# Optimization experiments

Measured on AMD Instinct MI355X. Metric: run time of the kernel, lower is better.

Reference implementation:

```python
import jax, jax.numpy as jnp
import numpy as np

B, S = 2, 1024
NH, NKV, HD = 32, 8, 128
Q_DIM, KV_DIM = NH * HD, NKV * HD
LEVEL = 256
ROPE_BASE = 10000.0


def fq_sym(x, level=LEVEL):
    # symmetric per-tensor fake quant with straight-through estimator
    qp = level // 2 - 1
    s = jnp.maximum(jax.lax.stop_gradient(jnp.max(jnp.abs(x))) / qp, 1e-8)
    q = jnp.clip(jnp.round(x / s), -qp, qp) * s
    return x + jax.lax.stop_gradient(q - x)


def fq_asym(x, level=LEVEL):
    # asymmetric (unsigned) fake quant for values in [0, 1]
    qp = level - 1
    s = jnp.maximum(jax.lax.stop_gradient(jnp.max(x)) / qp, 1e-8)
    q = jnp.clip(jnp.round(x / s), 0, qp) * s
    return x + jax.lax.stop_gradient(q - x)


def rope_tables(seq_len, dim):
    inv_freq = 1.0 / (ROPE_BASE ** (jnp.arange(0, dim, 2, dtype=jnp.float32) / dim))
    freqs = jnp.arange(seq_len, dtype=jnp.float32)[:, None] * inv_freq[None, :]  # [S, HD/2]
    emb = jnp.concatenate([freqs, freqs], axis=-1)  # [S, HD]
    return jnp.cos(emb), jnp.sin(emb)


def rotate_half(x):
    x1, x2 = jnp.split(x, 2, axis=-1)
    return jnp.concatenate([-x2, x1], axis=-1)


def setup_inputs() -> dict:
    key = jax.random.key(0)
    k1, k2, k3, k4 = jax.random.split(key, 4)
    d = Q_DIM + 2 * KV_DIM
    x = jax.random.normal(k1, (B, S, d), dtype=jnp.float32)
    w_qkv = jax.random.normal(k2, (d, d), dtype=jnp.float32) * (d ** -0.5)
    w_o = jax.random.normal(k3, (Q_DIM, Q_DIM), dtype=jnp.float32) * (Q_DIM ** -0.5)
    core_slope = jnp.float32(0.25)
    causal_mask = jnp.where(
        jnp.triu(jnp.ones((S, S), dtype=bool), k=1), jnp.float32(-1e9), jnp.float32(0.0)
    )[None, None]
    return {"x": x, "w_qkv": w_qkv, "w_o": w_o, "core_slope": core_slope,
            "causal_mask": causal_mask}


def reference(x, w_qkv, w_o, core_slope, causal_mask):
    qkv = jnp.einsum("bsd,ed->bse", x, w_qkv)  # Linear, no bias
    q = qkv[..., :Q_DIM].reshape(B, S, NH, HD).transpose(0, 2, 1, 3)
    k = qkv[..., Q_DIM:Q_DIM + KV_DIM].reshape(B, S, NKV, HD).transpose(0, 2, 1, 3)
    v = qkv[..., Q_DIM + KV_DIM:].reshape(B, S, NKV, HD).transpose(0, 2, 1, 3)
    q, k, v = fq_sym(q), fq_sym(k), fq_sym(v)
    cos, sin = rope_tables(S, HD)
    cos, sin = cos[None, None], sin[None, None]  # [1,1,S,HD]
    q = q * cos + rotate_half(q) * sin
    k = k * cos + rotate_half(k) * sin
    groups = NH // NKV
    if groups > 1:
        k = jnp.repeat(k, groups, axis=1)  # [B,NH,S,HD]
        v = jnp.repeat(v, groups, axis=1)
    scale = HD ** -0.5
    scores = jnp.einsum("bhqd,bhkd->bhqk", q, k) * scale
    scores = scores + causal_mask
    attn = jnp.clip(0.5 + core_slope * scores, 0.0, 1.0)  # UniAffineCore -> [0,1]
    attn = fq_asym(attn)
    out = jnp.einsum("bhqk,bhkd->bhqd", attn, v)
    out = fq_sym(out)
    out = out.transpose(0, 2, 1, 3).reshape(B, S, Q_DIM)
    out = jnp.einsum("bsd,ed->bse", out, w_o)
    return fq_sym(out)
```

## Files before the change

kernel.cpp:

```cpp
#include <hip/hip_runtime.h>
#include <stdint.h>

#define BB   2
#define SS   1024
#define NH   32
#define NKV  8
#define HD   128
#define DQ   4096
#define DKV  1024
#define DD   6144
#define MM   2048
#define SCALE 0.08838834764831845f

typedef __attribute__((ext_vector_type(8))) short short8;
typedef __attribute__((ext_vector_type(4))) float f4;

__device__ __forceinline__ float b2f(unsigned short b) {
    union { unsigned int u; float f; } v; v.u = ((unsigned int)b) << 16; return v.f;
}
__device__ __forceinline__ unsigned short f2b(float f) {
    union { float f; unsigned int u; } v; v.f = f;
    unsigned int u = v.u;
    unsigned int r = u + 0x7fffu + ((u >> 16) & 1u);
    return (unsigned short)(r >> 16);
}
__device__ __forceinline__ float fqs(float x, float s) {
    return fminf(fmaxf(rintf(x / s), -127.f), 127.f) * s;
}

typedef const unsigned int __attribute__((address_space(1)))* gas_ptr;
typedef unsigned int __attribute__((address_space(3)))* las_ptr;
__device__ __forceinline__ void gl_lds16(const void* g, void* l) {
    __builtin_amdgcn_global_load_lds((gas_ptr)(uintptr_t)g,
                                     (las_ptr)(unsigned int)(uintptr_t)l, 16, 0, 0);
}

__global__ void detect_kernel(const unsigned short* __restrict__ x, float* scal) {
    __shared__ float w[4];
    int tid = threadIdx.x;
    float m = 0.f;
    for (int i = tid; i < 65536; i += 256) m = fmaxf(m, fabsf(b2f(x[i])));
#pragma unroll
    for (int off = 32; off > 0; off >>= 1) m = fmaxf(m, __shfl_down(m, off));
    if ((tid & 63) == 0) w[tid >> 6] = m;
    __syncthreads();
    if (tid == 0) {
        float mm = fmaxf(fmaxf(w[0], w[1]), fmaxf(w[2], w[3]));
        scal[6] = (mm > 1e4f) ? 1.0f : 0.0f;
    }
}

__global__ void slope_kernel(const unsigned short* __restrict__ sp, float* scal) {
    if (threadIdx.x == 0)
        scal[7] = (scal[6] > 0.5f) ? ((const float*)sp)[0] : b2f(sp[0]);
}

__global__ void convert_split_kernel(const unsigned short* __restrict__ src,
                                     unsigned short* __restrict__ hi,
                                     unsigned short* __restrict__ lo,
                                     const float* __restrict__ scal) {
    size_t t = (size_t)blockIdx.x * 256 + threadIdx.x;
    float v[8] __attribute__((aligned(16)));
    if (scal[6] > 0.5f) {
        const float* s = (const float*)src + t * 8;
        *(float4*)(v)     = *(const float4*)(s);
        *(float4*)(v + 4) = *(const float4*)(s + 4);
    } else {
        unsigned short u[8] __attribute__((aligned(16)));
        *(uint4*)u = *(const uint4*)(src + t * 8);
#pragma unroll
        for (int i = 0; i < 8; i++) v[i] = b2f(u[i]);
    }
    unsigned short h8[8] __attribute__((aligned(16)));
    unsigned short l8[8] __attribute__((aligned(16)));
#pragma unroll
    for (int i = 0; i < 8; i++) {
        unsigned short h = f2b(v[i]);
        h8[i] = h;
        l8[i] = f2b(v[i] - b2f(h));
    }
    *(uint4*)(hi + t * 8) = *(uint4*)h8;
    *(uint4*)(lo + t * 8) = *(uint4*)l8;
}

template<int NT, int MODE>
__global__ __launch_bounds__(256, 2)
void gemm_hilo_kernel(const unsigned short* __restrict__ Ah,
                      const unsigned short* __restrict__ Al,
                      const unsigned short* __restrict__ Bh,
                      const unsigned short* __restrict__ Bl,
                      float* __restrict__ C,
                      int M, int N, int K,
                      float* __restrict__ scal)
{
    constexpr int PA    = 128 * 32;
    constexpr int OAL   = PA;
    constexpr int OBH   = (NT == 3) ? 2 * PA : PA;
    constexpr int OBL   = OBH + PA;
    constexpr int BUFSH = OBL + PA;
    __shared__ unsigned short lds[2 * BUFSH];
    __shared__ float wred[4];

    const int tid = threadIdx.x;
    const int bn = blockIdx.x << 7;
    const int bm = blockIdx.y << 7;
    const int wave = tid >> 6, lane = tid & 63;
    const int wm = (wave >> 1) << 6, wn = (wave & 1) << 6;
    const int lm = lane & 15, quad = lane >> 4;
    const int qx = quad ^ ((lm >> 1) & 3);

    const f4 z = {0.f, 0.f, 0.f, 0.f};
    f4 acc[4][4];
#pragma unroll
    for (int i = 0; i < 4; i++)
#pragma unroll
        for (int j = 0; j < 4; j++) acc[i][j] = z;

    const int r0 = tid >> 2;
    const int cs = ((tid & 3) ^ ((r0 >> 1) & 3)) * 8;
    const size_t ra0 = (size_t)(bm + r0) * K + cs;
    const size_t ra1 = (size_t)(bm + r0 + 64) * K + cs;
    const size_t rb0 = (size_t)(bn + r0) * K + cs;
    const size_t rb1 = (size_t)(bn + r0 + 64) * K + cs;
    const int l0 = tid * 8, l1 = (tid + 256) * 8;

    auto stage = [&](int bsel, int k0) {
        unsigned short* L = lds + bsel * BUFSH;
        gl_lds16(Ah + ra0 + k0, L + l0);
        gl_lds16(Ah + ra1 + k0, L + l1);
        if (NT == 3) {
            gl_lds16(Al + ra0 + k0, L + OAL + l0);
            gl_lds16(Al + ra1 + k0, L + OAL + l1);
        }
        gl_lds16(Bh + rb0 + k0, L + OBH + l0);
        gl_lds16(Bh + rb1 + k0, L + OBH + l1);
        gl_lds16(Bl + rb0 + k0, L + OBL + l0);
        gl_lds16(Bl + rb1 + k0, L + OBL + l1);
    };

    auto compute = [&](int bsel) {
        const unsigned short* L = lds + bsel * BUFSH;
        short8 a_h[4], b_h[4], b_l[4];
        short8 a_l[(NT == 3) ? 4 : 1];
#pragma unroll
        for (int t = 0; t < 4; t++) {
            int ro = (wm + t * 16 + lm) * 32 + qx * 8;
            a_h[t] = *(const short8*)(L + ro);
            if (NT == 3) a_l[t] = *(const short8*)(L + OAL + ro);
        }
#pragma unroll
        for (int t = 0; t < 4; t++) {
            int ro = (wn + t * 16 + lm) * 32 + qx * 8;
            b_h[t] = *(const short8*)(L + OBH + ro);
            b_l[t] = *(const short8*)(L + OBL + ro);
        }
#pragma unroll
        for (int i = 0; i < 4; i++)
#pragma unroll
            for (int j = 0; j < 4; j++) {
                acc[i][j] = __builtin_amdgcn_mfma_f32_16x16x32_bf16(a_h[i], b_h[j], acc[i][j], 0, 0, 0);
                if (NT == 3)
                    acc[i][j] = __builtin_amdgcn_mfma_f32_16x16x32_bf16(a_l[i], b_h[j], acc[i][j], 0, 0, 0);
                acc[i][j] = __builtin_amdgcn_mfma_f32_16x16x32_bf16(a_h[i], b_l[j], acc[i][j], 0, 0, 0);
            }
    };

#define WAITV do { if (NT == 3) asm volatile("s_waitcnt vmcnt(8)" ::: "memory"); \
                   else         asm volatile("s_waitcnt vmcnt(6)" ::: "memory"); } while (0)
#define WAIT0 asm volatile("s_waitcnt vmcnt(0)" ::: "memory")
#define SCHED0 __builtin_amdgcn_sched_barrier(0)
#define RBAR  __builtin_amdgcn_s_barrier()

    const int nt = K >> 5;
    stage(0, 0);
    stage(1, 32);
    for (int t = 0; t + 2 < nt; ++t) {
        WAITV;
        RBAR; SCHED0;
        compute(t & 1);
        SCHED0; RBAR; SCHED0;
        stage(t & 1, (t + 2) << 5);
    }
    WAITV;  RBAR; SCHED0; compute(nt & 1);
    WAIT0;  RBAR; SCHED0; compute((nt - 1) & 1);

#undef WAITV
#undef WAIT0
#undef SCHED0
#undef RBAR

    float mult = 1.f;
    if (MODE == 1) mult = fmaxf(scal[4] / 127.f, 1e-8f);
    float amax = 0.f;
#pragma unroll
    for (int i = 0; i < 4; i++)
#pragma unroll
        for (int j = 0; j < 4; j++)
#pragma unroll
            for (int r = 0; r < 4; r++) {
                float v = acc[i][j][r] * mult;
                amax = fmaxf(amax, fabsf(v));
                size_t row = (size_t)(bm + wm + i * 16 + quad * 4 + r);
                size_t col = (size_t)(bn + wn + j * 16 + lm);
                C[row * (size_t)N + col] = v;
            }
#pragma unroll
    for (int off = 32; off > 0; off >>= 1) amax = fmaxf(amax, __shfl_down(amax, off));
    if (lane == 0) wred[wave] = amax;
    __syncthreads();
    if (tid == 0) {
        float m = fmaxf(fmaxf(wred[0], wred[1]), fmaxf(wred[2], wred[3]));
        int slot = (MODE == 0) ? ((bn < 4096) ? 0 : ((bn < 5120) ? 1 : 2)) : 5;
        atomicMax((unsigned int*)(scal + slot), __float_as_uint(m));
    }
}

__global__ void quant_rope_hilo_kernel(const float* __restrict__ qkv,
                                       unsigned short* __restrict__ Qh,
                                       unsigned short* __restrict__ Ql,
                                       unsigned short* __restrict__ Kh,
                                       unsigned short* __restrict__ Kl,
                                       unsigned short* __restrict__ Vc,
                                       const float* __restrict__ scal)
{
    int t = blockIdx.x * 256 + threadIdx.x;
    int f = t * 8;
    int r = f / DD;
    int c = f - r * DD;
    int b = r >> 10, sp = r & 1023;
    const float* src = qkv + (size_t)r * DD + c;
    float x[8] __attribute__((aligned(16)));
    *(float4*)(x)     = *(const float4*)(src);
    *(float4*)(x + 4) = *(const float4*)(src + 4);

    if (c < 5120) {
        float s; int d; unsigned short *dh, *dl;
        if (c < 4096) {
            s = fmaxf(scal[0] / 127.f, 1e-8f);
            int head = c >> 7; d = c & 127;
            size_t off = (((size_t)(b * NH + head) * SS + sp) << 7) + d;
            dh = Qh + off; dl = Ql + off;
        } else {
            int cc = c - 4096;
            s = fmaxf(scal[1] / 127.f, 1e-8f);
            int head = cc >> 7; d = cc & 127;
            size_t off = (((size_t)(b * NKV + head) * SS + sp) << 7) + d;
            dh = Kh + off; dl = Kl + off;
        }
        int cp = (d < 64) ? (c + 64) : (c - 64);
        float sgn = (d < 64) ? -1.f : 1.f;
        const float* psrc = qkv + (size_t)r * DD + cp;
        float p[8] __attribute__((aligned(16)));
        *(float4*)(p)     = *(const float4*)(psrc);
        *(float4*)(p + 4) = *(const float4*)(psrc + 4);
        unsigned short h8[8] __attribute__((aligned(16)));
        unsigned short l8[8] __attribute__((aligned(16)));
#pragma unroll
        for (int i = 0; i < 8; i++) {
            float xq = fqs(x[i], s);
            float pq = fqs(p[i], s);
            int fi = (d + i) & 63;
            float inv = expf((float)fi * -0.14391156831212787f);
            float ang = (float)sp * inv;
            float sn, cs;
            sincosf(ang, &sn, &cs);
            float o = xq * cs + sgn * pq * sn;
            unsigned short hb = f2b(o);
            h8[i] = hb;
            l8[i] = f2b(o - b2f(hb));
        }
        *(uint4*)(dh) = *(uint4*)h8;
        *(uint4*)(dl) = *(uint4*)l8;
    } else {
        int cc = c - 5120;
        float s = fmaxf(scal[2] / 127.f, 1e-8f);
        int head = cc >> 7, d = cc & 127;
        unsigned short* dst = Vc + (((size_t)(b * NKV + head) * SS + sp) << 7) + d;
        unsigned short o8[8] __attribute__((aligned(16)));
#pragma unroll
        for (int i = 0; i < 8; i++) {
            float code = fminf(fmaxf(rintf(x[i] / s), -127.f), 127.f);
            o8[i] = f2b(code);
        }
        *(uint4*)(dst) = *(uint4*)o8;
    }
}

__global__ void vtrans_kernel(const unsigned short* __restrict__ Vc,
                              unsigned short* __restrict__ Vt)
{
    __shared__ __attribute__((aligned(16))) unsigned short L[64][72];
    const int dtile = blockIdx.x;
    const int ktile = blockIdx.y;
    const int bh    = blockIdx.z;
    const int tid = threadIdx.x;
#pragma unroll
    for (int it = 0; it < 2; it++) {
        int lin = it * 256 + tid;
        int row = lin >> 3, c8 = (lin & 7) * 8;
        *(uint4*)&L[row][c8] =
            *(const uint4*)(Vc + ((size_t)bh * SS + ktile * 64 + row) * HD + dtile * 64 + c8);
    }
    __syncthreads();
#pragma unroll
    for (int it = 0; it < 2; it++) {
        int lin = it * 256 + tid;
        int dr = lin >> 3, k8 = (lin & 7) * 8;
        unsigned short o8[8] __attribute__((aligned(16)));
#pragma unroll
        for (int i = 0; i < 8; i++) o8[i] = L[k8 + i][dr];
        *(uint4*)(Vt + ((size_t)bh * HD + dtile * 64 + dr) * SS + ktile * 64 + k8) = *(uint4*)o8;
    }
}

template<int PASS>
__global__ __launch_bounds__(256, 2)
void attn_mfma_kernel(const unsigned short* __restrict__ Qh,
                      const unsigned short* __restrict__ Ql,
                      const unsigned short* __restrict__ Kh,
                      const unsigned short* __restrict__ Kl,
                      const unsigned short* __restrict__ Vt,
                      float* __restrict__ O,
                      float* __restrict__ scal)
{
    __shared__ __attribute__((aligned(16))) unsigned short Ps[PASS ? 4 : 1][16][72];
    __shared__ float wred[4];
    const int x = blockIdx.x;
    const int qc = x & 15, h = (x >> 4) & 31, b = x >> 9;
    const int hk = h >> 2;
    const int tid = threadIdx.x;
    const int wave = tid >> 6, lane = tid & 63;
    const int lm = lane & 15, quad = lane >> 4;
    const float coef = scal[7] * SCALE;
    float s_a = 1.f, s_av = 1.f;
    if (PASS) {
        s_a = fmaxf(scal[3] / 255.f, 1e-8f);
        float s_v = fmaxf(scal[2] / 127.f, 1e-8f);
        s_av = s_a * s_v;
    }

    const size_t qbase = ((size_t)((b * NH + h) * SS) + qc * 64 + wave * 16 + lm) * HD + quad * 8;
    short8 qh[4], ql[4];
#pragma unroll
    for (int kk = 0; kk < 4; kk++) {
        qh[kk] = *(const short8*)(Qh + qbase + kk * 32);
        ql[kk] = *(const short8*)(Ql + qbase + kk * 32);
    }
    const size_t kbase = (size_t)((b * NKV + hk) * SS) * HD + quad * 8;
    const size_t vbase = (size_t)((b * NKV + hk) * HD) * SS + quad * 8;

    const f4 z = {0.f, 0.f, 0.f, 0.f};
    f4 oacc[8];
    if (PASS) {
#pragma unroll
        for (int j2 = 0; j2 < 8; j2++) oacc[j2] = z;
    }
    float amax = 0.f;
    const int qg = qc * 64 + wave * 16 + quad * 4;

    for (int kt = 0; kt <= qc; kt++) {
        f4 acc[4];
#pragma unroll
        for (int j = 0; j < 4; j++) acc[j] = z;
        __builtin_amdgcn_s_setprio(1);
#pragma unroll
        for (int j = 0; j < 4; j++) {
            const size_t kb = kbase + (size_t)(kt * 64 + j * 16 + lm) * HD;
#pragma unroll
            for (int kk = 0; kk < 4; kk++) {
                short8 kh8 = *(const short8*)(Kh + kb + kk * 32);
                short8 kl8 = *(const short8*)(Kl + kb + kk * 32);
                acc[j] = __builtin_amdgcn_mfma_f32_16x16x32_bf16(qh[kk], kh8, acc[j], 0, 0, 0);
                acc[j] = __builtin_amdgcn_mfma_f32_16x16x32_bf16(ql[kk], kh8, acc[j], 0, 0, 0);
                acc[j] = __builtin_amdgcn_mfma_f32_16x16x32_bf16(qh[kk], kl8, acc[j], 0, 0, 0);
            }
        }
        __builtin_amdgcn_s_setprio(0);
        const bool diag = (kt == qc);
#pragma unroll
        for (int j = 0; j < 4; j++) {
            int kg = kt * 64 + j * 16 + lm;
#pragma unroll
            for (int r = 0; r < 4; r++) {
                bool ok = (!diag) || (kg <= qg + r);
                float a = 0.5f + coef * acc[j][r];
                a = fminf(fmaxf(a, 0.f), 1.f);
                if (PASS == 0) {
                    if (ok) amax = fmaxf(amax, a);
                } else {
                    float cd = ok ? fminf(rintf(a / s_a), 255.f) : 0.f;
                    Ps[wave][quad * 4 + r][j * 16 + lm] = f2b(cd);
                }
            }
        }
        if (PASS) {
            short8 pa0 = *(const short8*)&Ps[wave][lm][quad * 8];
            short8 pa1 = *(const short8*)&Ps[wave][lm][32 + quad * 8];
            __builtin_amdgcn_s_setprio(1);
#pragma unroll
            for (int j2 = 0; j2 < 8; j2++) {
                const unsigned short* vp = Vt + vbase + (size_t)(j2 * 16 + lm) * SS + kt * 64;
                short8 v0 = *(const short8*)(vp);
                short8 v1 = *(const short8*)(vp + 32);
                oacc[j2] = __builtin_amdgcn_mfma_f32_16x16x32_bf16(pa0, v0, oacc[j2], 0, 0, 0);
                oacc[j2] = __builtin_amdgcn_mfma_f32_16x16x32_bf16(pa1, v1, oacc[j2], 0, 0, 0);
            }
            __builtin_amdgcn_s_setprio(0);
        }
    }

    if (PASS == 0) {
#pragma unroll
        for (int off = 32; off > 0; off >>= 1) amax = fmaxf(amax, __shfl_down(amax, off));
        if (lane == 0) wred[wave] = amax;
        __syncthreads();
        if (tid == 0) {
            float m = fmaxf(fmaxf(wred[0], wred[1]), fmaxf(wred[2], wred[3]));
            atomicMax((unsigned int*)(scal + 3), __float_as_uint(m));
        }
    } else {
        float am = 0.f;
        const size_t orow = (size_t)(b * SS + qc * 64 + wave * 16 + quad * 4);
#pragma unroll
        for (int j2 = 0; j2 < 8; j2++)
#pragma unroll
            for (int r = 0; r < 4; r++) {
                float v = oacc[j2][r] * s_av;
                am = fmaxf(am, fabsf(v));
                O[(orow + r) * DQ + h * HD + j2 * 16 + lm] = v;
            }
#pragma unroll
        for (int off = 32; off > 0; off >>= 1) am = fmaxf(am, __shfl_down(am, off));
        if (lane == 0) wred[wave] = am;
        __syncthreads();
        if (tid == 0) {
            float m = fmaxf(fmaxf(wred[0], wred[1]), fmaxf(wred[2], wred[3]));
            atomicMax((unsigned int*)(scal + 4), __float_as_uint(m));
        }
    }
}

__global__ void quant_o_codes_kernel(const float* __restrict__ O,
                                     const float* __restrict__ scal,
                                     unsigned short* __restrict__ Oq)
{
    size_t t = (size_t)blockIdx.x * 256 + threadIdx.x;
    float s = fmaxf(scal[4] / 127.f, 1e-8f);
    float4 v = *(const float4*)(O + t * 4);
    unsigned short o[4] __attribute__((aligned(8)));
    o[0] = f2b(fminf(fmaxf(rintf(v.x / s), -127.f), 127.f));
    o[1] = f2b(fminf(fmaxf(rintf(v.y / s), -127.f), 127.f));
    o[2] = f2b(fminf(fmaxf(rintf(v.z / s), -127.f), 127.f));
    o[3] = f2b(fminf(fmaxf(rintf(v.w / s), -127.f), 127.f));
    *(uint2*)(Oq + t * 4) = *(uint2*)o;
}

__global__ void final_q_kernel(const float* __restrict__ X,
                               const float* __restrict__ scal,
                               float* __restrict__ out)
{
    size_t t = (size_t)blockIdx.x * 256 + threadIdx.x;
    float s = fmaxf(scal[5] / 127.f, 1e-8f);
    float4 v = *(const float4*)(X + t * 4);
    float4 o;
    o.x = fqs(v.x, s);
    o.y = fqs(v.y, s);
    o.z = fqs(v.z, s);
    o.w = fqs(v.w, s);
    *(float4*)(out + t * 4) = o;
}

extern "C" void kernel_launch(void* const* d_in, const int* in_sizes, int n_in,
                              void* d_out, int out_size, void* d_ws, size_t ws_size,
                              hipStream_t stream)
{
    const unsigned short* x      = (const unsigned short*)d_in[0];
    const unsigned short* w_qkv  = (const unsigned short*)d_in[1];
    const unsigned short* w_o    = (const unsigned short*)d_in[2];
    const unsigned short* slope  = (const unsigned short*)d_in[3];
    (void)in_sizes; (void)n_in; (void)out_size; (void)ws_size;

    char* ws = (char*)d_ws;
    float* scal          = (float*)ws;
    unsigned short* xh   = (unsigned short*)(ws + 256);
    unsigned short* xl   = (unsigned short*)(ws + 25166080);
    unsigned short* wqh  = (unsigned short*)(ws + 50331904);
    unsigned short* wql  = (unsigned short*)(ws + 125829376);
    float* qkv           = (float*)(ws + 201326848);
    unsigned short* Qh   = (unsigned short*)(ws + 251658496);
    unsigned short* Ql   = (unsigned short*)(ws + 268435712);
    unsigned short* Kh   = (unsigned short*)(ws + 285212928);
    unsigned short* Kl   = (unsigned short*)(ws + 289407232);
    unsigned short* Vt   = (unsigned short*)(ws + 293601536);
    unsigned short* Vc   = (unsigned short*)(ws + 297795840);
    unsigned short* woh  = (unsigned short*)(ws + 256);
    unsigned short* wol  = (unsigned short*)(ws + 33554688);
    float* O             = (float*)(ws + 67109376);
    unsigned short* Oqc  = (unsigned short*)(ws + 100663808);
    float* out2          = (float*)(ws + 201326848);
    float* outp          = (float*)d_out;

    hipMemsetAsync(scal, 0, 256, stream);
    detect_kernel<<<1, 256, 0, stream>>>(x, scal);
    slope_kernel<<<1, 64, 0, stream>>>(slope, scal);
    convert_split_kernel<<<6144, 256, 0, stream>>>(x, xh, xl, scal);
    convert_split_kernel<<<18432, 256, 0, stream>>>(w_qkv, wqh, wql, scal);
    gemm_hilo_kernel<3, 0><<<dim3(48, 16), 256, 0, stream>>>(xh, xl, wqh, wql, qkv,
                                                             MM, DD, DD, scal);
    quant_rope_hilo_kernel<<<6144, 256, 0, stream>>>(qkv, Qh, Ql, Kh, Kl, Vc, scal);
    vtrans_kernel<<<dim3(2, 16, 16), 256, 0, stream>>>(Vc, Vt);
    convert_split_kernel<<<8192, 256, 0, stream>>>(w_o, woh, wol, scal);
    attn_mfma_kernel<0><<<1024, 256, 0, stream>>>(Qh, Ql, Kh, Kl, Vt, O, scal);
    attn_mfma_kernel<1><<<1024, 256, 0, stream>>>(Qh, Ql, Kh, Kl, Vt, O, scal);
    quant_o_codes_kernel<<<8192, 256, 0, stream>>>(O, scal, Oqc);
    gemm_hilo_kernel<2, 1><<<dim3(32, 16), 256, 0, stream>>>(Oqc, Oqc, woh, wol, out2,
                                                             MM, DQ, DQ, scal);
    final_q_kernel<<<8192, 256, 0, stream>>>(out2, scal, outp);
}
```

Baseline: 1.591 ms.

## Materialize attention scores to scratch and simplify GEMM to single-buffered LDS

The two-pass attention, which recomputed QK^T in both passes, is split into a score kernel and a PV kernel. The score kernel writes raw causal scores to a packed scratch buffer of about 140 MB and reduces the attention max. The PV kernel reads those scores back, quantizes them and multiplies by V. Both attention kernels walk query chunks in reverse order so the longest causal rows are scheduled first. Separately, the hi/lo GEMM drops its double-buffered async-copy pipeline for a single LDS buffer with __syncthreads and asks for 4 blocks per CU. That trades load/compute overlap for occupancy and risks exposing memory latency in the dominant GEMMs, while the score scratch adds heavy HBM traffic in exchange for skipping the QK recompute.

New measurement: 1.455 ms. 1.09x faster.

```diff
diff --git a/kernel.cpp b/kernel.cpp
--- a/kernel.cpp
+++ b/kernel.cpp
@@ -84,7 +84,7 @@
 }
 
 template<int NT, int MODE>
-__global__ __launch_bounds__(256, 2)
+__global__ __launch_bounds__(256, 4)
 void gemm_hilo_kernel(const unsigned short* __restrict__ Ah,
                       const unsigned short* __restrict__ Al,
                       const unsigned short* __restrict__ Bh,
@@ -97,8 +97,7 @@
     constexpr int OAL   = PA;
     constexpr int OBH   = (NT == 3) ? 2 * PA : PA;
     constexpr int OBL   = OBH + PA;
-    constexpr int BUFSH = OBL + PA;
-    __shared__ unsigned short lds[2 * BUFSH];
+    __shared__ unsigned short lds[OBL + PA];
     __shared__ float wred[4];
 
     const int tid = threadIdx.x;
@@ -124,35 +123,31 @@
     const size_t rb1 = (size_t)(bn + r0 + 64) * K + cs;
     const int l0 = tid * 8, l1 = (tid + 256) * 8;
 
-    auto stage = [&](int bsel, int k0) {
-        unsigned short* L = lds + bsel * BUFSH;
-        gl_lds16(Ah + ra0 + k0, L + l0);
-        gl_lds16(Ah + ra1 + k0, L + l1);
+    for (int k0 = 0; k0 < K; k0 += 32) {
+        gl_lds16(Ah + ra0 + k0, lds + l0);
+        gl_lds16(Ah + ra1 + k0, lds + l1);
         if (NT == 3) {
-            gl_lds16(Al + ra0 + k0, L + OAL + l0);
-            gl_lds16(Al + ra1 + k0, L + OAL + l1);
-        }
-        gl_lds16(Bh + rb0 + k0, L + OBH + l0);
-        gl_lds16(Bh + rb1 + k0, L + OBH + l1);
-        gl_lds16(Bl + rb0 + k0, L + OBL + l0);
-        gl_lds16(Bl + rb1 + k0, L + OBL + l1);
-    };
-
-    auto compute = [&](int bsel) {
-        const unsigned short* L = lds + bsel * BUFSH;
+            gl_lds16(Al + ra0 + k0, lds + OAL + l0);
+            gl_lds16(Al + ra1 + k0, lds + OAL + l1);
+        }
+        gl_lds16(Bh + rb0 + k0, lds + OBH + l0);
+        gl_lds16(Bh + rb1 + k0, lds + OBH + l1);
+        gl_lds16(Bl + rb0 + k0, lds + OBL + l0);
+        gl_lds16(Bl + rb1 + k0, lds + OBL + l1);
+        __syncthreads();
         short8 a_h[4], b_h[4], b_l[4];
         short8 a_l[(NT == 3) ? 4 : 1];
 #pragma unroll
         for (int t = 0; t < 4; t++) {
             int ro = (wm + t * 16 + lm) * 32 + qx * 8;
-            a_h[t] = *(const short8*)(L + ro);
-            if (NT == 3) a_l[t] = *(const short8*)(L + OAL + ro);
+            a_h[t] = *(const short8*)(lds + ro);
+            if (NT == 3) a_l[t] = *(const short8*)(lds + OAL + ro);
         }
 #pragma unroll
         for (int t = 0; t < 4; t++) {
             int ro = (wn + t * 16 + lm) * 32 + qx * 8;
-            b_h[t] = *(const short8*)(L + OBH + ro);
-            b_l[t] = *(const short8*)(L + OBL + ro);
+            b_h[t] = *(const short8*)(lds + OBH + ro);
+            b_l[t] = *(const short8*)(lds + OBL + ro);
         }
 #pragma unroll
         for (int i = 0; i < 4; i++)
@@ -163,31 +158,8 @@
                     acc[i][j] = __builtin_amdgcn_mfma_f32_16x16x32_bf16(a_l[i], b_h[j], acc[i][j], 0, 0, 0);
                 acc[i][j] = __builtin_amdgcn_mfma_f32_16x16x32_bf16(a_h[i], b_l[j], acc[i][j], 0, 0, 0);
             }
-    };
-
-#define WAITV do { if (NT == 3) asm volatile("s_waitcnt vmcnt(8)" ::: "memory"); \
-                   else         asm volatile("s_waitcnt vmcnt(6)" ::: "memory"); } while (0)
-#define WAIT0 asm volatile("s_waitcnt vmcnt(0)" ::: "memory")
-#define SCHED0 __builtin_amdgcn_sched_barrier(0)
-#define RBAR  __builtin_amdgcn_s_barrier()
-
-    const int nt = K >> 5;
-    stage(0, 0);
-    stage(1, 32);
-    for (int t = 0; t + 2 < nt; ++t) {
-        WAITV;
-        RBAR; SCHED0;
-        compute(t & 1);
-        SCHED0; RBAR; SCHED0;
-        stage(t & 1, (t + 2) << 5);
-    }
-    WAITV;  RBAR; SCHED0; compute(nt & 1);
-    WAIT0;  RBAR; SCHED0; compute((nt - 1) & 1);
-
-#undef WAITV
-#undef WAIT0
-#undef SCHED0
-#undef RBAR
+        __syncthreads();
+    }
 
     float mult = 1.f;
     if (MODE == 1) mult = fmaxf(scal[4] / 127.f, 1e-8f);
@@ -313,31 +285,23 @@
     }
 }
 
-template<int PASS>
 __global__ __launch_bounds__(256, 2)
-void attn_mfma_kernel(const unsigned short* __restrict__ Qh,
-                      const unsigned short* __restrict__ Ql,
-                      const unsigned short* __restrict__ Kh,
-                      const unsigned short* __restrict__ Kl,
-                      const unsigned short* __restrict__ Vt,
-                      float* __restrict__ O,
-                      float* __restrict__ scal)
-{
-    __shared__ __attribute__((aligned(16))) unsigned short Ps[PASS ? 4 : 1][16][72];
+void attn_score_kernel(const unsigned short* __restrict__ Qh,
+                       const unsigned short* __restrict__ Ql,
+                       const unsigned short* __restrict__ Kh,
+                       const unsigned short* __restrict__ Kl,
+                       float* __restrict__ Scr,
+                       float* __restrict__ scal)
+{
     __shared__ float wred[4];
     const int x = blockIdx.x;
-    const int qc = x & 15, h = (x >> 4) & 31, b = x >> 9;
+    const int qc = 15 - (x & 15);
+    const int h = (x >> 4) & 31, b = x >> 9;
     const int hk = h >> 2;
     const int tid = threadIdx.x;
     const int wave = tid >> 6, lane = tid & 63;
     const int lm = lane & 15, quad = lane >> 4;
     const float coef = scal[7] * SCALE;
-    float s_a = 1.f, s_av = 1.f;
-    if (PASS) {
-        s_a = fmaxf(scal[3] / 255.f, 1e-8f);
-        float s_v = fmaxf(scal[2] / 127.f, 1e-8f);
-        s_av = s_a * s_v;
-    }
 
     const size_t qbase = ((size_t)((b * NH + h) * SS) + qc * 64 + wave * 16 + lm) * HD + quad * 8;
     short8 qh[4], ql[4];
@@ -347,14 +311,9 @@
         ql[kk] = *(const short8*)(Ql + qbase + kk * 32);
     }
     const size_t kbase = (size_t)((b * NKV + hk) * SS) * HD + quad * 8;
-    const size_t vbase = (size_t)((b * NKV + hk) * HD) * SS + quad * 8;
+    const size_t scrbase = ((size_t)(b * NH + h) * 136 + (size_t)(qc * (qc + 1) / 2)) * 4096;
 
     const f4 z = {0.f, 0.f, 0.f, 0.f};
-    f4 oacc[8];
-    if (PASS) {
-#pragma unroll
-        for (int j2 = 0; j2 < 8; j2++) oacc[j2] = z;
-    }
     float amax = 0.f;
     const int qg = qc * 64 + wave * 16 + quad * 4;
 
@@ -377,66 +336,119 @@
         }
         __builtin_amdgcn_s_setprio(0);
         const bool diag = (kt == qc);
+        float* st = Scr + scrbase + (size_t)kt * 4096;
 #pragma unroll
         for (int j = 0; j < 4; j++) {
             int kg = kt * 64 + j * 16 + lm;
 #pragma unroll
             for (int r = 0; r < 4; r++) {
+                float sv = acc[j][r];
+                st[(wave * 16 + quad * 4 + r) * 64 + j * 16 + lm] = sv;
                 bool ok = (!diag) || (kg <= qg + r);
-                float a = 0.5f + coef * acc[j][r];
-                a = fminf(fmaxf(a, 0.f), 1.f);
-                if (PASS == 0) {
-                    if (ok) amax = fmaxf(amax, a);
-                } else {
-                    float cd = ok ? fminf(rintf(a / s_a), 255.f) : 0.f;
-                    Ps[wave][quad * 4 + r][j * 16 + lm] = f2b(cd);
+                if (ok) {
+                    float a = 0.5f + coef * sv;
+                    a = fminf(fmaxf(a, 0.f), 1.f);
+                    amax = fmaxf(amax, a);
                 }
             }
         }
-        if (PASS) {
-            short8 pa0 = *(const short8*)&Ps[wave][lm][quad * 8];
-            short8 pa1 = *(const short8*)&Ps[wave][lm][32 + quad * 8];
-            __builtin_amdgcn_s_setprio(1);
-#pragma unroll
-            for (int j2 = 0; j2 < 8; j2++) {
-                const unsigned short* vp = Vt + vbase + (size_t)(j2 * 16 + lm) * SS + kt * 64;
-                short8 v0 = *(const short8*)(vp);
-                short8 v1 = *(const short8*)(vp + 32);
-                oacc[j2] = __builtin_amdgcn_mfma_f32_16x16x32_bf16(pa0, v0, oacc[j2], 0, 0, 0);
-                oacc[j2] = __builtin_amdgcn_mfma_f32_16x16x32_bf16(pa1, v1, oacc[j2], 0, 0, 0);
-            }
-            __builtin_amdgcn_s_setprio(0);
-        }
-    }
-
-    if (PASS == 0) {
-#pragma unroll
-        for (int off = 32; off > 0; off >>= 1) amax = fmaxf(amax, __shfl_down(amax, off));
-        if (lane == 0) wred[wave] = amax;
-        __syncthreads();
-        if (tid == 0) {
-            float m = fmaxf(fmaxf(wred[0], wred[1]), fmaxf(wred[2], wred[3]));
-            atomicMax((unsigned int*)(scal + 3), __float_as_uint(m));
-        }
-    } else {
-        float am = 0.f;
-        const size_t orow = (size_t)(b * SS + qc * 64 + wave * 16 + quad * 4);
-#pragma unroll
-        for (int j2 = 0; j2 < 8; j2++)
-#pragma unroll
-            for (int r = 0; r < 4; r++) {
-                float v = oacc[j2][r] * s_av;
-                am = fmaxf(am, fabsf(v));
-                O[(orow + r) * DQ + h * HD + j2 * 16 + lm] = v;
-            }
-#pragma unroll
-        for (int off = 32; off > 0; off >>= 1) am = fmaxf(am, __shfl_down(am, off));
-        if (lane == 0) wred[wave] = am;
-        __syncthreads();
-        if (tid == 0) {
-            float m = fmaxf(fmaxf(wred[0], wred[1]), fmaxf(wred[2], wred[3]));
-            atomicMax((unsigned int*)(scal + 4), __float_as_uint(m));
-        }
+    }
+
+#pragma unroll
+    for (int off = 32; off > 0; off >>= 1) amax = fmaxf(amax, __shfl_down(amax, off));
+    if (lane == 0) wred[wave] = amax;
+    __syncthreads();
+    if (tid == 0) {
+        float m = fmaxf(fmaxf(wred[0], wred[1]), fmaxf(wred[2], wred[3]));
+        atomicMax((unsigned int*)(scal + 3), __float_as_uint(m));
+    }
+}
+
+__global__ __launch_bounds__(256, 4)
+void attn_pv_kernel(const float* __restrict__ Scr,
+                    const unsigned short* __restrict__ Vt,
+                    float* __restrict__ O,
+                    float* __restrict__ scal)
+{
+    __shared__ float wred[4];
+    const int x = blockIdx.x;
+    const int qc = 15 - (x & 15);
+    const int h = (x >> 4) & 31, b = x >> 9;
+    const int hk = h >> 2;
+    const int tid = threadIdx.x;
+    const int wave = tid >> 6, lane = tid & 63;
+    const int lm = lane & 15, quad = lane >> 4;
+    const float coef = scal[7] * SCALE;
+    const float s_a = fmaxf(scal[3] / 255.f, 1e-8f);
+    const float s_v = fmaxf(scal[2] / 127.f, 1e-8f);
+    const float s_av = s_a * s_v;
+
+    const size_t vbase = (size_t)((b * NKV + hk) * HD) * SS + quad * 8;
+    const size_t scrbase = ((size_t)(b * NH + h) * 136 + (size_t)(qc * (qc + 1) / 2)) * 4096
+                         + (size_t)(wave * 16 + lm) * 64 + quad * 8;
+    const int qg = qc * 64 + wave * 16 + lm;
+
+    const f4 z = {0.f, 0.f, 0.f, 0.f};
+    f4 oacc[8];
+#pragma unroll
+    for (int j2 = 0; j2 < 8; j2++) oacc[j2] = z;
+
+    for (int kt = 0; kt <= qc; kt++) {
+        const float* sp = Scr + scrbase + (size_t)kt * 4096;
+        float sc[16] __attribute__((aligned(16)));
+        *(float4*)(sc)      = *(const float4*)(sp);
+        *(float4*)(sc + 4)  = *(const float4*)(sp + 4);
+        *(float4*)(sc + 8)  = *(const float4*)(sp + 32);
+        *(float4*)(sc + 12) = *(const float4*)(sp + 36);
+        const bool diag = (kt == qc);
+        unsigned short cd[16] __attribute__((aligned(16)));
+#pragma unroll
+        for (int i = 0; i < 8; i++) {
+            int kg = kt * 64 + quad * 8 + i;
+            bool ok = (!diag) || (kg <= qg);
+            float a = 0.5f + coef * sc[i];
+            a = fminf(fmaxf(a, 0.f), 1.f);
+            cd[i] = f2b(ok ? fminf(rintf(a / s_a), 255.f) : 0.f);
+        }
+#pragma unroll
+        for (int i = 0; i < 8; i++) {
+            int kg = kt * 64 + 32 + quad * 8 + i;
+            bool ok = (!diag) || (kg <= qg);
+            float a = 0.5f + coef * sc[8 + i];
+            a = fminf(fmaxf(a, 0.f), 1.f);
+            cd[8 + i] = f2b(ok ? fminf(rintf(a / s_a), 255.f) : 0.f);
+        }
+        short8 pa0 = *(const short8*)(cd);
+        short8 pa1 = *(const short8*)(cd + 8);
+        __builtin_amdgcn_s_setprio(1);
+#pragma unroll
+        for (int j2 = 0; j2 < 8; j2++) {
+            const unsigned short* vp = Vt + vbase + (size_t)(j2 * 16 + lm) * SS + kt * 64;
+            short8 v0 = *(const short8*)(vp);
+            short8 v1 = *(const short8*)(vp + 32);
+            oacc[j2] = __builtin_amdgcn_mfma_f32_16x16x32_bf16(pa0, v0, oacc[j2], 0, 0, 0);
+            oacc[j2] = __builtin_amdgcn_mfma_f32_16x16x32_bf16(pa1, v1, oacc[j2], 0, 0, 0);
+        }
+        __builtin_amdgcn_s_setprio(0);
+    }
+
+    float am = 0.f;
+    const size_t orow = (size_t)(b * SS + qc * 64 + wave * 16 + quad * 4);
+#pragma unroll
+    for (int j2 = 0; j2 < 8; j2++)
+#pragma unroll
+        for (int r = 0; r < 4; r++) {
+            float v = oacc[j2][r] * s_av;
+            am = fmaxf(am, fabsf(v));
+            O[(orow + r) * DQ + h * HD + j2 * 16 + lm] = v;
+        }
+#pragma unroll
+    for (int off = 32; off > 0; off >>= 1) am = fmaxf(am, __shfl_down(am, off));
+    if (lane == 0) wred[wave] = am;
+    __syncthreads();
+    if (tid == 0) {
+        float m = fmaxf(fmaxf(wred[0], wred[1]), fmaxf(wred[2], wred[3]));
+        atomicMax((unsigned int*)(scal + 4), __float_as_uint(m));
     }
 }
 
@@ -496,6 +508,7 @@
     unsigned short* woh  = (unsigned short*)(ws + 256);
     unsigned short* wol  = (unsigned short*)(ws + 33554688);
     float* O             = (float*)(ws + 67109376);
+    float* Scr           = (float*)(ws + 100663808);
     unsigned short* Oqc  = (unsigned short*)(ws + 100663808);
     float* out2          = (float*)(ws + 201326848);
     float* outp          = (float*)d_out;
@@ -510,8 +523,8 @@
     quant_rope_hilo_kernel<<<6144, 256, 0, stream>>>(qkv, Qh, Ql, Kh, Kl, Vc, scal);
     vtrans_kernel<<<dim3(2, 16, 16), 256, 0, stream>>>(Vc, Vt);
     convert_split_kernel<<<8192, 256, 0, stream>>>(w_o, woh, wol, scal);
-    attn_mfma_kernel<0><<<1024, 256, 0, stream>>>(Qh, Ql, Kh, Kl, Vt, O, scal);
-    attn_mfma_kernel<1><<<1024, 256, 0, stream>>>(Qh, Ql, Kh, Kl, Vt, O, scal);
+    attn_score_kernel<<<1024, 256, 0, stream>>>(Qh, Ql, Kh, Kl, Scr, scal);
+    attn_pv_kernel<<<1024, 256, 0, stream>>>(Scr, Vt, O, scal);
     quant_o_codes_kernel<<<8192, 256, 0, stream>>>(O, scal, Oqc);
     gemm_hilo_kernel<2, 1><<<dim3(32, 16), 256, 0, stream>>>(Oqc, Oqc, woh, wol, out2,
                                                              MM, DQ, DQ, scal);
```
